# Kernel optimization log

Measured on AMD Instinct MI355X. Metric: run time of the kernel, lower is better.

## Reference

```python
import jax, jax.numpy as jnp
import numpy as np

N, K, IN_DIMS, OUT_DIMS = 50000, 32, 256, 256


def _he(key, shape):
    fan_in = int(np.prod(shape[:-1]))
    std = 1.0 / np.sqrt(fan_in)
    return jax.random.uniform(key, shape, minval=-std, maxval=std, dtype=jnp.float32)


def setup_inputs() -> dict:
    key = jax.random.key(0)
    kx, kadj, kedge, k1, k2, k3, k4 = jax.random.split(key, 7)
    return {
        "x": jax.random.normal(kx, (N, IN_DIMS), dtype=jnp.float32),
        "adj": jax.random.randint(kadj, (N, K), 0, N),
        "edge": jax.random.normal(kedge, (N, K, 2), dtype=jnp.float32),
        "Wc": _he(k1, (IN_DIMS, OUT_DIMS)),
        "Wn": _he(k2, (IN_DIMS, OUT_DIMS)),
        "We": _he(k3, (2, OUT_DIMS)),
        "q": _he(k4, (OUT_DIMS, 1)),
        "b": jnp.zeros((OUT_DIMS,), dtype=jnp.float32),
        "training": 0,
    }


def reference(x, adj, edge, Wc, Wn, We, q, b, training):
    Zc = x @ Wc                                   # [N, D]
    v_Wn = x @ Wn                                 # [N, D]
    e_We = jnp.einsum('nke,ed->nkd', edge, We)    # [N, K, D]
    # -1 entries in adj are padding; count valid neighbors per node
    nh_sizes = jnp.count_nonzero(adj + 1, axis=1).astype(jnp.float32)[:, None]  # [N, 1]
    neighbor = v_Wn[adj] + e_We                   # [N, K, D] gather + edge proj
    # softmax over the trailing size-1 axis, exactly as in the source
    weight = jax.nn.softmax(jnp.einsum('nkd,do->nko', neighbor, q), axis=-1)  # [N, K, 1]
    Zn = jnp.sum(neighbor * weight, axis=1) / jnp.maximum(nh_sizes, 1.0)      # [N, D]
    h = jax.nn.relu(Zn + Zc + b)
    # training=0 -> no dropout (deterministic inference path)
    return h
```

## Files before the change

kernel.cpp:

```cpp
#include <hip/hip_runtime.h>
#include <hip/hip_bf16.h>
#include <stdint.h>

#define N_NODES 50000
#define KNB 32
#define DIM 256

typedef short s8v __attribute__((ext_vector_type(8)));
typedef float f4v __attribute__((ext_vector_type(4)));
typedef float f2v __attribute__((ext_vector_type(2)));
typedef int i4v __attribute__((ext_vector_type(4)));
typedef unsigned short u16;
typedef unsigned char u8;

__device__ inline float bf2f(u16 h) {
    unsigned int u = ((unsigned int)h) << 16;
    return __builtin_bit_cast(float, u);
}
__device__ inline u16 f2bf(float f) {
    unsigned int u = __builtin_bit_cast(unsigned int, f);
    unsigned int r = (u + 0x7fffu + ((u >> 16) & 1u)) >> 16;
    return (u16)r;
}

__device__ inline unsigned fp8_enc1_manual(float f) {
    unsigned fb = __builtin_bit_cast(unsigned, f);
    unsigned s = (fb >> 24) & 0x80u;
    float a = fminf(fabsf(f), 448.0f);
    unsigned u = __builtin_bit_cast(unsigned, a * 0x1p-120f);
    unsigned r = (u + 0x7ffffu + ((u >> 20) & 1u)) >> 20;
    return s | r;
}

template <bool HI>
__device__ inline unsigned fp8_enc_pair(float f0, float f1, unsigned old) {
#if __has_builtin(__builtin_amdgcn_cvt_pk_fp8_f32)
    return (unsigned)__builtin_amdgcn_cvt_pk_fp8_f32(f0, f1, (int)old, HI);
#else
    unsigned half = fp8_enc1_manual(f0) | (fp8_enc1_manual(f1) << 8);
    return HI ? ((old & 0x0000ffffu) | (half << 16))
              : ((old & 0xffff0000u) | half);
#endif
}

template <bool HI>
__device__ inline f2v fp8_dec_pair(unsigned w) {
#if __has_builtin(__builtin_amdgcn_cvt_pk_f32_fp8)
    return __builtin_amdgcn_cvt_pk_f32_fp8(w, HI);
#else
    unsigned h0 = (w >> (HI ? 16 : 0)) & 0xffu;
    unsigned h1 = (w >> (HI ? 24 : 8)) & 0xffu;
    f2v r;
    r[0] = __builtin_bit_cast(float, ((h0 & 0x80u) << 24) | ((h0 & 0x7fu) << 20)) * 0x1p+120f;
    r[1] = __builtin_bit_cast(float, ((h1 & 0x80u) << 24) | ((h1 & 0x7fu) << 20)) * 0x1p+120f;
    return r;
#endif
}

#define GLOAD16(gp, lp) __builtin_amdgcn_global_load_lds( \
    (const __attribute__((address_space(1))) unsigned int*)(gp), \
    (__attribute__((address_space(3))) unsigned int*)(lp), 16, 0, 0)


__global__ __launch_bounds__(256) void k_convert(
    const float* __restrict__ x, const float* __restrict__ Wc,
    const float* __restrict__ Wn, const float* __restrict__ edge,
    const int* __restrict__ adj, u16* __restrict__ xbs, u8* __restrict__ xq,
    u16* __restrict__ Wct, u16* __restrict__ Wnt, float* __restrict__ esc,
    u16* __restrict__ adj16, float* __restrict__ invv)
{
    int64_t tid = (int64_t)blockIdx.x * blockDim.x + threadIdx.x;
    int64_t stride = (int64_t)gridDim.x * blockDim.x;

    const int64_t nitems = (int64_t)N_NODES * 16;
    for (int64_t i = tid; i < nitems; i += stride) {
        int n = (int)(i >> 4), d16 = (int)(i & 15);
        const float4* xp = (const float4*)(x + (int64_t)n * 256 + d16 * 16);
        float4 t0 = xp[0], t1 = xp[1], t2 = xp[2], t3 = xp[3];
        float v[16] = {t0.x, t0.y, t0.z, t0.w, t1.x, t1.y, t1.z, t1.w,
                       t2.x, t2.y, t2.z, t2.w, t3.x, t3.y, t3.z, t3.w};
        u16* bp = xbs + ((int64_t)(d16 >> 1) * N_NODES + n) * 32 + (d16 & 1) * 16;
        s8v b0, b1;
        #pragma unroll
        for (int j = 0; j < 8; ++j) {
            b0[j] = (short)f2bf(v[j]);
            b1[j] = (short)f2bf(v[j + 8]);
        }
        *(s8v*)bp = b0;
        *(s8v*)(bp + 8) = b1;

        unsigned q0, q1, q2, q3;
        q0 = fp8_enc_pair<false>(v[0], v[1], 0);   q0 = fp8_enc_pair<true>(v[2], v[3], q0);
        q1 = fp8_enc_pair<false>(v[4], v[5], 0);   q1 = fp8_enc_pair<true>(v[6], v[7], q1);
        q2 = fp8_enc_pair<false>(v[8], v[9], 0);   q2 = fp8_enc_pair<true>(v[10], v[11], q2);
        q3 = fp8_enc_pair<false>(v[12], v[13], 0); q3 = fp8_enc_pair<true>(v[14], v[15], q3);
        u8* qp = xq + ((int64_t)(d16 >> 2) * N_NODES + n) * 64 + (d16 & 3) * 16;
        i4v qv = {(int)q0, (int)q1, (int)q2, (int)q3};
        *(i4v*)qp = qv;
    }

    for (int64_t i = tid; i < 256 * 256; i += stride) {
        int r = (int)(i >> 8), c = (int)(i & 255);
        Wct[c * 256 + r] = f2bf(Wc[i]);
        Wnt[c * 256 + r] = f2bf(Wn[i]);
    }

    int lane = threadIdx.x & 63;
    int gw = (int)((blockIdx.x * 256 + threadIdx.x) >> 6);
    int nwaves = (int)((gridDim.x * 256) >> 6);
    for (int n = gw; n < N_NODES; n += nwaves) {
        float ev = edge[(int64_t)n * 64 + lane];
        ev += __shfl_xor(ev, 2);
        ev += __shfl_xor(ev, 4);
        ev += __shfl_xor(ev, 8);
        ev += __shfl_xor(ev, 16);
        ev += __shfl_xor(ev, 32);
        int a = (lane < 32) ? adj[n * 32 + lane] : 0;
        unsigned long long m = __ballot(lane < 32 && a != -1);
        float inv = 1.0f / fmaxf((float)__popcll(m), 1.0f);
        if (lane < 32) {
            int w = a < 0 ? a + N_NODES : a;
            adj16[n * 32 + lane] = (u16)w;
        }
        if (lane < 2) esc[n * 2 + lane] = ev * inv;
        if (lane == 0) invv[n] = inv;
    }
}

__global__ __launch_bounds__(256) void k_gather(
    const u8* __restrict__ xq, const u16* __restrict__ adj16,
    const float* __restrict__ invv, u16* __restrict__ sbs)
{
    int wv = threadIdx.x >> 6, lane = threadIdx.x & 63;
    int c = blockIdx.x & 3;
    int n0 = (int)(blockIdx.x >> 2) * 64 + wv * 16;
    if (n0 >= N_NODES) return;
    int node = lane >> 2, seg = lane & 3;
    int n = n0 + node;
    int nc = n < N_NODES ? n : N_NODES - 1;

    int64_t aoff = (int64_t)n0 * 32 + lane * 8;
    int4 aw = *(const int4*)(adj16 + aoff);
    int a[8];
    a[0] = aw.x & 0xffff; a[1] = (int)(((unsigned)aw.x) >> 16);
    a[2] = aw.y & 0xffff; a[3] = (int)(((unsigned)aw.y) >> 16);
    a[4] = aw.z & 0xffff; a[5] = (int)(((unsigned)aw.z) >> 16);
    a[6] = aw.w & 0xffff; a[7] = (int)(((unsigned)aw.w) >> 16);

    float iv = invv[nc];
    const u8* base = xq + (int64_t)c * N_NODES * 64 + seg * 16;

    float acc[16];
    #pragma unroll
    for (int j = 0; j < 16; ++j) acc[j] = 0.f;

    #pragma unroll
    for (int k = 0; k < 32; ++k) {
        int src = (lane & 60) | (k >> 3);
        int idx = __shfl(a[k & 7], src);
        i4v w = *(const i4v*)(base + (int64_t)idx * 64);
        #pragma unroll
        for (int r = 0; r < 4; ++r) {
            f2v lo = fp8_dec_pair<false>((unsigned)w[r]);
            f2v hi = fp8_dec_pair<true>((unsigned)w[r]);
            acc[r * 4 + 0] += lo[0];
            acc[r * 4 + 1] += lo[1];
            acc[r * 4 + 2] += hi[0];
            acc[r * 4 + 3] += hi[1];
        }
    }

    if (n < N_NODES) {
        int c8 = c * 2 + (seg >> 1);
        u16* sp = sbs + ((int64_t)c8 * N_NODES + n) * 32 + (seg & 1) * 16;
        s8v o0, o1;
        #pragma unroll
        for (int j = 0; j < 8; ++j) {
            o0[j] = (short)f2bf(acc[j] * iv);
            o1[j] = (short)f2bf(acc[j + 8] * iv);
        }
        *(s8v*)sp = o0;
        *(s8v*)(sp + 8) = o1;
    }
}

__device__ inline void stage_A32(u16* tile, const u16* src, int row0,
                                 int chunk, int wv, int lane)
{
    #pragma unroll
    for (int cc = 0; cc < 2; ++cc) {
        int idxbase = cc * 256 + wv * 64;
        int idx = idxbase + lane;
        int row = idx >> 2, seg = idx & 3;
        int gr = row0 + row; if (gr >= N_NODES) gr = N_NODES - 1;
        int srcseg = seg ^ ((row ^ (row >> 2)) & 3);
        const u16* g = src + ((int64_t)chunk * N_NODES + gr) * 32 + srcseg * 8;
        GLOAD16(g, (char*)tile + idxbase * 16);
    }
}
__device__ inline void stage_B32(u16* tile, const u16* src, int col0,
                                 int kofsEl, int wv, int lane)
{
    #pragma unroll
    for (int cc = 0; cc < 2; ++cc) {
        int idxbase = cc * 256 + wv * 64;
        int idx = idxbase + lane;
        int row = idx >> 2, seg = idx & 3;
        int srcseg = seg ^ ((row ^ (row >> 2)) & 3);
        const u16* g = src + (int64_t)(col0 + row) * 256 + kofsEl + srcseg * 8;
        GLOAD16(g, (char*)tile + idxbase * 16);
    }
}

__global__ __launch_bounds__(256, 4) void k_gemm(
    const u16* __restrict__ xbs, const u16* __restrict__ sbs,
    const u16* __restrict__ Wct, const u16* __restrict__ Wnt,
    const float* __restrict__ esc, const float* __restrict__ We,
    const float* __restrict__ bias, float* __restrict__ out)
{
    __shared__ u16 Atile[2][128 * 32];
    __shared__ u16 Btile[2][128 * 32];

    int wv = threadIdx.x >> 6, lane = threadIdx.x & 63;
    int wm = wv >> 1, wn = wv & 1;
    int bm = blockIdx.x >> 1;
    int nt = blockIdx.x & 1;
    int mrow0 = bm * 128;
    int ncol0 = nt * 128;

    f4v acc[4][4];
    #pragma unroll
    for (int m = 0; m < 4; ++m)
        #pragma unroll
        for (int n = 0; n < 4; ++n) acc[m][n] = (f4v){0.f, 0.f, 0.f, 0.f};

    stage_A32(Atile[0], xbs, mrow0, 0, wv, lane);
    stage_B32(Btile[0], Wct, ncol0, 0, wv, lane);
    __syncthreads();

    int cur = 0;
    int lrow = wm * 64, lcol = wn * 64;
    int l15 = lane & 15, l4 = lane >> 4;

    for (int kb = 0; kb < 16; ++kb) {
        if (kb < 15) {
            int kn = kb + 1;
            const u16* As = (kn < 8) ? xbs : sbs;
            const u16* Bs = (kn < 8) ? Wct : Wnt;
            stage_A32(Atile[cur ^ 1], As, mrow0, kn & 7, wv, lane);
            stage_B32(Btile[cur ^ 1], Bs, ncol0, (kn & 7) * 32, wv, lane);
        }
        const u16* At = Atile[cur];
        const u16* Bt = Btile[cur];
        s8v af[4], bfr[4];
        #pragma unroll
        for (int m = 0; m < 4; ++m) {
            int row = lrow + m * 16 + l15;
            int sg = (l4 ^ ((row ^ (row >> 2)) & 3)) * 16;
            af[m] = *(const s8v*)((const char*)At + row * 64 + sg);
        }
        #pragma unroll
        for (int n = 0; n < 4; ++n) {
            int col = lcol + n * 16 + l15;
            int sg = (l4 ^ ((col ^ (col >> 2)) & 3)) * 16;
            bfr[n] = *(const s8v*)((const char*)Bt + col * 64 + sg);
        }
        #pragma unroll
        for (int m = 0; m < 4; ++m)
            #pragma unroll
            for (int n = 0; n < 4; ++n)
                acc[m][n] = __builtin_amdgcn_mfma_f32_16x16x32_bf16(
                    af[m], bfr[n], acc[m][n], 0, 0, 0);
        __syncthreads();
        cur ^= 1;
    }

    #pragma unroll
    for (int m = 0; m < 4; ++m) {
        int r0 = mrow0 + lrow + m * 16 + l4 * 4;
        float e0[4], e1[4];
        #pragma unroll
        for (int r = 0; r < 4; ++r) {
            int row = r0 + r; if (row >= N_NODES) row = N_NODES - 1;
            e0[r] = esc[row * 2];
            e1[r] = esc[row * 2 + 1];
        }
        #pragma unroll
        for (int n = 0; n < 4; ++n) {
            int col = ncol0 + lcol + n * 16 + l15;
            float bc = bias[col];
            float w0 = We[col];
            float w1 = We[256 + col];
            #pragma unroll
            for (int r = 0; r < 4; ++r) {
                int row = r0 + r;
                if (row < N_NODES) {
                    float v = acc[m][n][r] + bc + e0[r] * w0 + e1[r] * w1;
                    out[(int64_t)row * 256 + col] = fmaxf(v, 0.0f);
                }
            }
        }
    }
}

extern "C" void kernel_launch(void* const* d_in, const int* in_sizes, int n_in,
                              void* d_out, int out_size, void* d_ws, size_t ws_size,
                              hipStream_t stream) {
    const float* x    = (const float*)d_in[0];
    const int*   adj  = (const int*)d_in[1];
    const float* edge = (const float*)d_in[2];
    const float* Wc   = (const float*)d_in[3];
    const float* Wn   = (const float*)d_in[4];
    const float* We   = (const float*)d_in[5];
    const float* bias = (const float*)d_in[7];
    float* out = (float*)d_out;

    char* ws = (char*)d_ws;
    u16*   xbs   = (u16*)(ws);
    u16*   sbs   = (u16*)(ws + 25600000);
    float* esc   = (float*)(ws + 51200000);
    u16*   Wct   = (u16*)(ws + 51600000);
    u16*   Wnt   = (u16*)(ws + 51731072);
    u16*   adj16 = (u16*)(ws + 51862144);
    float* invv  = (float*)(ws + 55062144);
    u8*    xq    = (u8*)(ws + 55262144);

    k_convert<<<2048, 256, 0, stream>>>(x, Wc, Wn, edge, adj, xbs, xq, Wct, Wnt,
                                        esc, adj16, invv);
    k_gather<<<((N_NODES + 63) / 64) * 4, 256, 0, stream>>>(xq, adj16, invv, sbs);
    k_gemm<<<(N_NODES + 127) / 128 * 2, 256, 0, stream>>>(xbs, sbs, Wct, Wnt, esc, We, bias, out);
}
```

Before: 92.08 us.

## Split gather across 8 lanes per node and remap GEMM blocks by XCD

```diff
diff --git a/kernel.cpp b/kernel.cpp
--- a/kernel.cpp
+++ b/kernel.cpp
@@ -10,6 +10,7 @@
 typedef float f4v __attribute__((ext_vector_type(4)));
 typedef float f2v __attribute__((ext_vector_type(2)));
 typedef int i4v __attribute__((ext_vector_type(4)));
+typedef int i2v __attribute__((ext_vector_type(2)));
 typedef unsigned short u16;
 typedef unsigned char u8;
 
@@ -133,34 +134,29 @@
 {
     int wv = threadIdx.x >> 6, lane = threadIdx.x & 63;
     int c = blockIdx.x & 3;
-    int n0 = (int)(blockIdx.x >> 2) * 64 + wv * 16;
+    int n0 = (int)(blockIdx.x >> 2) * 32 + wv * 8;
     if (n0 >= N_NODES) return;
-    int node = lane >> 2, seg = lane & 3;
+    int node = lane >> 3, seg = lane & 7;
     int n = n0 + node;
     int nc = n < N_NODES ? n : N_NODES - 1;
 
-    int64_t aoff = (int64_t)n0 * 32 + lane * 8;
-    int4 aw = *(const int4*)(adj16 + aoff);
-    int a[8];
-    a[0] = aw.x & 0xffff; a[1] = (int)(((unsigned)aw.x) >> 16);
-    a[2] = aw.y & 0xffff; a[3] = (int)(((unsigned)aw.y) >> 16);
-    a[4] = aw.z & 0xffff; a[5] = (int)(((unsigned)aw.z) >> 16);
-    a[6] = aw.w & 0xffff; a[7] = (int)(((unsigned)aw.w) >> 16);
+    int64_t aoff = (int64_t)n0 * 32 + lane * 4;
+    i2v aw = *(const i2v*)(adj16 + aoff);
+    int a[4];
+    a[0] = aw[0] & 0xffff; a[1] = (int)(((unsigned)aw[0]) >> 16);
+    a[2] = aw[1] & 0xffff; a[3] = (int)(((unsigned)aw[1]) >> 16);
 
     float iv = invv[nc];
-    const u8* base = xq + (int64_t)c * N_NODES * 64 + seg * 16;
-
-    float acc[16];
-    #pragma unroll
-    for (int j = 0; j < 16; ++j) acc[j] = 0.f;
-
+    const u8* base = xq + (int64_t)c * N_NODES * 64 + seg * 8;
+
+    float acc[8] = {0.f, 0.f, 0.f, 0.f, 0.f, 0.f, 0.f, 0.f};
     #pragma unroll
     for (int k = 0; k < 32; ++k) {
-        int src = (lane & 60) | (k >> 3);
-        int idx = __shfl(a[k & 7], src);
-        i4v w = *(const i4v*)(base + (int64_t)idx * 64);
-        #pragma unroll
-        for (int r = 0; r < 4; ++r) {
+        int src = (lane & 56) | (k >> 2);
+        int idx = __shfl(a[k & 3], src);
+        i2v w = *(const i2v*)(base + (int64_t)idx * 64);
+        #pragma unroll
+        for (int r = 0; r < 2; ++r) {
             f2v lo = fp8_dec_pair<false>((unsigned)w[r]);
             f2v hi = fp8_dec_pair<true>((unsigned)w[r]);
             acc[r * 4 + 0] += lo[0];
@@ -171,16 +167,12 @@
     }
 
     if (n < N_NODES) {
-        int c8 = c * 2 + (seg >> 1);
-        u16* sp = sbs + ((int64_t)c8 * N_NODES + n) * 32 + (seg & 1) * 16;
-        s8v o0, o1;
-        #pragma unroll
-        for (int j = 0; j < 8; ++j) {
-            o0[j] = (short)f2bf(acc[j] * iv);
-            o1[j] = (short)f2bf(acc[j + 8] * iv);
-        }
-        *(s8v*)sp = o0;
-        *(s8v*)(sp + 8) = o1;
+        int c8 = c * 2 + (seg >> 2);
+        u16* sp = sbs + ((int64_t)c8 * N_NODES + n) * 32 + (seg & 3) * 8;
+        s8v o;
+        #pragma unroll
+        for (int j = 0; j < 8; ++j) o[j] = (short)f2bf(acc[j] * iv);
+        *(s8v*)sp = o;
     }
 }
 
@@ -223,8 +215,14 @@
 
     int wv = threadIdx.x >> 6, lane = threadIdx.x & 63;
     int wm = wv >> 1, wn = wv & 1;
-    int bm = blockIdx.x >> 1;
-    int nt = blockIdx.x & 1;
+
+    int nwg = gridDim.x;
+    int xcd = blockIdx.x & 7, lo = blockIdx.x >> 3;
+    int q = nwg >> 3, r = nwg & 7;
+    int bid = (xcd < r ? xcd * (q + 1) : r * (q + 1) + (xcd - r) * q) + lo;
+
+    int bm = bid >> 1;
+    int nt = bid & 1;
     int mrow0 = bm * 128;
     int ncol0 = nt * 128;
 
@@ -280,10 +278,10 @@
         int r0 = mrow0 + lrow + m * 16 + l4 * 4;
         float e0[4], e1[4];
         #pragma unroll
-        for (int r = 0; r < 4; ++r) {
-            int row = r0 + r; if (row >= N_NODES) row = N_NODES - 1;
-            e0[r] = esc[row * 2];
-            e1[r] = esc[row * 2 + 1];
+        for (int r2 = 0; r2 < 4; ++r2) {
+            int row = r0 + r2; if (row >= N_NODES) row = N_NODES - 1;
+            e0[r2] = esc[row * 2];
+            e1[r2] = esc[row * 2 + 1];
         }
         #pragma unroll
         for (int n = 0; n < 4; ++n) {
@@ -292,10 +290,10 @@
             float w0 = We[col];
             float w1 = We[256 + col];
             #pragma unroll
-            for (int r = 0; r < 4; ++r) {
-                int row = r0 + r;
+            for (int r2 = 0; r2 < 4; ++r2) {
+                int row = r0 + r2;
                 if (row < N_NODES) {
-                    float v = acc[m][n][r] + bc + e0[r] * w0 + e1[r] * w1;
+                    float v = acc[m][n][r2] + bc + e0[r2] * w0 + e1[r2] * w1;
                     out[(int64_t)row * 256 + col] = fmaxf(v, 0.0f);
                 }
             }
@@ -327,6 +325,6 @@
 
     k_convert<<<2048, 256, 0, stream>>>(x, Wc, Wn, edge, adj, xbs, xq, Wct, Wnt,
                                         esc, adj16, invv);
-    k_gather<<<((N_NODES + 63) / 64) * 4, 256, 0, stream>>>(xq, adj16, invv, sbs);
+    k_gather<<<((N_NODES + 31) / 32) * 4, 256, 0, stream>>>(xq, adj16, invv, sbs);
     k_gemm<<<(N_NODES + 127) / 128 * 2, 256, 0, stream>>>(xbs, sbs, Wct, Wnt, esc, We, bias, out);
 }
```

Result: faster. 87.47 us (median of 2 runs) (-5.0%).
